# Kernel optimization log

Measured on AMD Instinct MI355X. Metric: run time of the kernel, lower is better.

Reference implementation:

```python
import jax, jax.numpy as jnp
import numpy as np

S1, S2, B, H, E, IN, OUT, NL = 8, 32, 256, 1024, 512, 2, 2, 4


def setup_inputs() -> dict:
    key = jax.random.key(0)
    ks = jax.random.split(key, 20)
    s_h = 1.0 / np.sqrt(H)
    inp = {
        'input': jax.random.normal(ks[0], (B, IN), jnp.float32),
        'h0': jax.random.normal(ks[1], (NL, B, H), jnp.float32) * 0.5,
        'c0': jax.random.normal(ks[2], (NL, B, H), jnp.float32) * 0.5,
        'all_outputs': jax.random.normal(ks[3], (S1, S2, B, H), jnp.float32),
        'W_emb': jax.random.normal(ks[4], (E, IN), jnp.float32) / np.sqrt(IN),
        'b_emb': jax.random.normal(ks[5], (E,), jnp.float32) * 0.01,
        'W_attn': jax.random.normal(ks[6], (1, 2 * H), jnp.float32) / np.sqrt(2 * H),
        'b_attn': jax.random.normal(ks[7], (1,), jnp.float32) * 0.01,
        'Wih0': jax.random.normal(ks[8], (4 * H, E + H), jnp.float32) / np.sqrt(E + H),
        'Whh0': jax.random.normal(ks[9], (4 * H, H), jnp.float32) * s_h,
        'bih0': jax.random.normal(ks[10], (4 * H,), jnp.float32) * 0.01,
        'bhh0': jax.random.normal(ks[11], (4 * H,), jnp.float32) * 0.01,
        'Wih_r': jax.random.normal(ks[12], (NL - 1, 4 * H, H), jnp.float32) * s_h,
        'Whh_r': jax.random.normal(ks[13], (NL - 1, 4 * H, H), jnp.float32) * s_h,
        'bih_r': jax.random.normal(ks[14], (NL - 1, 4 * H), jnp.float32) * 0.01,
        'bhh_r': jax.random.normal(ks[15], (NL - 1, 4 * H), jnp.float32) * 0.01,
        'W_out': jax.random.normal(ks[16], (OUT, H), jnp.float32) * s_h,
        'b_out': jax.random.normal(ks[17], (OUT,), jnp.float32) * 0.01,
    }
    return inp


def _lstm_cell(x, h, c, Wih, Whh, bih, bhh):
    g = x @ Wih.T + h @ Whh.T + bih + bhh  # [B, 4H], torch gate order i,f,g,o
    i, f, gg, o = jnp.split(g, 4, axis=1)
    c2 = jax.nn.sigmoid(f) * c + jax.nn.sigmoid(i) * jnp.tanh(gg)
    h2 = jax.nn.sigmoid(o) * jnp.tanh(c2)
    return h2, c2


def reference(input, h0, c0, all_outputs, W_emb, b_emb, W_attn, b_attn,
              Wih0, Whh0, bih0, bhh0, Wih_r, Whh_r, bih_r, bhh_r, W_out, b_out):
    s1, s2, b, h_dim = all_outputs.shape
    # embedding (dropout = identity in eval mode)
    embedded = jax.nn.relu(input @ W_emb.T + b_emb)  # [B, E]
    h_top = h0[0]  # [B, H]
    # attn(cat(h_top, y)) decomposed: h part is shared across all (j, i)
    w_h = W_attn[0, :h_dim]
    w_y = W_attn[0, h_dim:]
    scores = (jnp.einsum('jibh,h->jib', all_outputs, w_y)
              + (h_top @ w_h)[None, None, :] + b_attn[0])  # [S1, S2, B]
    # torch cats per-(j,i) [B,1] columns j-major -> [B, S1*S2]
    normalized = jax.nn.softmax(scores.reshape(s1 * s2, b).T, axis=1)  # [B, S1*S2]
    temp = normalized.reshape(b, s1, s2)
    # NOTE: original writes into an expand()-ed zero buffer, so every j-slice
    # aliases the same memory; after the loop all slices equal the last j's bmm
    # result and sum(0) multiplies it by S1. We replicate that exactly.
    applied_last = jnp.einsum('bi,ibh->bh', temp[:, -1, :], all_outputs[-1])  # [B, H]
    final_attn = s1 * applied_last
    x = jnp.concatenate([final_attn, embedded], axis=1)  # [B, H+E]
    hs, cs = [], []
    h, c = _lstm_cell(x, h0[0], c0[0], Wih0, Whh0, bih0, bhh0)
    hs.append(h); cs.append(c)
    for l in range(Wih_r.shape[0]):  # inter-layer dropout = identity in eval
        h, c = _lstm_cell(h, h0[l + 1], c0[l + 1], Wih_r[l], Whh_r[l], bih_r[l], bhh_r[l])
        hs.append(h); cs.append(c)
    h_new = jnp.stack(hs)
    c_new = jnp.stack(cs)
    final_output = h @ W_out.T + b_out  # [B, OUT]
    return final_output, h_new, c_new, normalized
```

## Files before the change

### kernel.cpp

```cpp
#include <hip/hip_runtime.h>
#include <hip/hip_bf16.h>

typedef __bf16 bf16x8 __attribute__((ext_vector_type(8)));
typedef __bf16 bf16x4 __attribute__((ext_vector_type(4)));
typedef float  f32x4  __attribute__((ext_vector_type(4)));

#define O_FINAL 0
#define O_H     512
#define O_C     1049088
#define O_NORM  2097664

__device__ __forceinline__ bf16x8 cvt8(float4 a, float4 b) {
  bf16x8 r;
  r[0] = (__bf16)a.x; r[1] = (__bf16)a.y; r[2] = (__bf16)a.z; r[3] = (__bf16)a.w;
  r[4] = (__bf16)b.x; r[5] = (__bf16)b.y; r[6] = (__bf16)b.z; r[7] = (__bf16)b.w;
  return r;
}

template<int K>
__device__ __forceinline__ void tile_gemm_bb(const __bf16* __restrict__ A,
                                             const __bf16* __restrict__ W,
                                             int r0, int j0, char* lds,
                                             f32x4 acc[2]) {
  constexpr int NK = K / 64;
  constexpr int D = 4;
  const int t = threadIdx.x, lane = t & 63, wave = t >> 6;
  const int rf = wave & 3, gg = wave >> 2;
  const int tr = t >> 3, chunk = t & 7;
  const __bf16* wsrc = W + (size_t)((tr >> 4) * 1024 + j0 + (tr & 15)) * K + chunk * 8;
  const __bf16* asrc = A + (size_t)(r0 + tr) * K + chunk * 8;
  const int sw_off = (chunk ^ (tr & 7)) << 4;
  const int woff = 8192 + tr * 128 + sw_off;
  const int aoff = tr * 128 + sw_off;
  const int a_tr  = rf * 16 + (lane & 15);
  const int w_tr0 = gg * 32 + (lane & 15);
  const int w_tr1 = w_tr0 + 16;
  const int ksel  = lane >> 4;

  bf16x8 wp[D], ap[D];
#pragma unroll
  for (int d = 0; d < D; ++d) {
    wp[d] = *(const bf16x8*)(wsrc + d * 64);
    ap[d] = *(const bf16x8*)(asrc + d * 64);
  }
#pragma unroll
  for (int s = 0; s < NK; ++s) {
    const int sl = s % D;
    char* buf = lds + (s & 1) * 16384;
    *(bf16x8*)(buf + aoff) = ap[sl];
    *(bf16x8*)(buf + woff) = wp[sl];
    if (s + D < NK) {
      wp[sl] = *(const bf16x8*)(wsrc + (s + D) * 64);
      ap[sl] = *(const bf16x8*)(asrc + (s + D) * 64);
    }
    __syncthreads();
#pragma unroll
    for (int s2 = 0; s2 < 2; ++s2) {
      const int chk = s2 * 4 + ksel;
      bf16x8 af  = *(const bf16x8*)(buf + a_tr * 128 + ((chk ^ (a_tr & 7)) << 4));
      bf16x8 wf0 = *(const bf16x8*)(buf + 8192 + w_tr0 * 128 + ((chk ^ (w_tr0 & 7)) << 4));
      bf16x8 wf1 = *(const bf16x8*)(buf + 8192 + w_tr1 * 128 + ((chk ^ (w_tr1 & 7)) << 4));
      acc[0] = __builtin_amdgcn_mfma_f32_16x16x32_bf16(af, wf0, acc[0], 0, 0, 0);
      acc[1] = __builtin_amdgcn_mfma_f32_16x16x32_bf16(af, wf1, acc[1], 0, 0, 0);
    }
  }
}

template<int K>
__device__ __forceinline__ void tile_gemm_ff(const float* __restrict__ A,
                                             const float* __restrict__ W,
                                             int r0, int j0, char* lds,
                                             f32x4 acc[2]) {
  constexpr int NK = K / 64;
  constexpr int D = 4;
  const int t = threadIdx.x, lane = t & 63, wave = t >> 6;
  const int rf = wave & 3, gg = wave >> 2;
  const int tr = t >> 3, chunk = t & 7;
  const float* wsrc = W + (size_t)((tr >> 4) * 1024 + j0 + (tr & 15)) * K + chunk * 8;
  const float* asrc = A + (size_t)(r0 + tr) * K + chunk * 8;
  const int sw_off = (chunk ^ (tr & 7)) << 4;
  const int woff = 8192 + tr * 128 + sw_off;
  const int aoff = tr * 128 + sw_off;
  const int a_tr  = rf * 16 + (lane & 15);
  const int w_tr0 = gg * 32 + (lane & 15);
  const int w_tr1 = w_tr0 + 16;
  const int ksel  = lane >> 4;

  float4 wp[D][2], ap[D][2];
#pragma unroll
  for (int d = 0; d < D; ++d) {
    wp[d][0] = *(const float4*)(wsrc + d * 64);
    wp[d][1] = *(const float4*)(wsrc + d * 64 + 4);
    ap[d][0] = *(const float4*)(asrc + d * 64);
    ap[d][1] = *(const float4*)(asrc + d * 64 + 4);
  }
#pragma unroll
  for (int s = 0; s < NK; ++s) {
    const int sl = s % D;
    char* buf = lds + (s & 1) * 16384;
    *(bf16x8*)(buf + aoff) = cvt8(ap[sl][0], ap[sl][1]);
    *(bf16x8*)(buf + woff) = cvt8(wp[sl][0], wp[sl][1]);
    if (s + D < NK) {
      wp[sl][0] = *(const float4*)(wsrc + (s + D) * 64);
      wp[sl][1] = *(const float4*)(wsrc + (s + D) * 64 + 4);
      ap[sl][0] = *(const float4*)(asrc + (s + D) * 64);
      ap[sl][1] = *(const float4*)(asrc + (s + D) * 64 + 4);
    }
    __syncthreads();
#pragma unroll
    for (int s2 = 0; s2 < 2; ++s2) {
      const int chk = s2 * 4 + ksel;
      bf16x8 af  = *(const bf16x8*)(buf + a_tr * 128 + ((chk ^ (a_tr & 7)) << 4));
      bf16x8 wf0 = *(const bf16x8*)(buf + 8192 + w_tr0 * 128 + ((chk ^ (w_tr0 & 7)) << 4));
      bf16x8 wf1 = *(const bf16x8*)(buf + 8192 + w_tr1 * 128 + ((chk ^ (w_tr1 & 7)) << 4));
      acc[0] = __builtin_amdgcn_mfma_f32_16x16x32_bf16(af, wf0, acc[0], 0, 0, 0);
      acc[1] = __builtin_amdgcn_mfma_f32_16x16x32_bf16(af, wf1, acc[1], 0, 0, 0);
    }
  }
}

__global__ __launch_bounds__(512) void k_front(
    const float* __restrict__ AO, const float* __restrict__ Wattn,
    float* __restrict__ sc,
    const float* __restrict__ h0,
    const float* __restrict__ Whh0, const float* __restrict__ Whh_r,
    const float* __restrict__ bih0, const float* __restrict__ bhh0,
    const float* __restrict__ bih_r, const float* __restrict__ bhh_r,
    float* __restrict__ Gh,
    const float* __restrict__ Wih0, const float* __restrict__ Wih_r,
    __bf16* __restrict__ Wihb) {
  const int t = threadIdx.x, lane = t & 63, wave = t >> 6;
  if (blockIdx.x < 2048) {
    const float* wy = Wattn + 1024;
    float4 wv[4];
#pragma unroll
    for (int q = 0; q < 4; ++q) wv[q] = *(const float4*)(wy + lane * 4 + 256 * q);
    const int row0 = (blockIdx.x * 8 + wave) * 4;
    float a4[4];
#pragma unroll
    for (int rr = 0; rr < 4; ++rr) {
      const float4* rp = (const float4*)(AO + (size_t)(row0 + rr) * 1024);
      float a = 0.f;
#pragma unroll
      for (int q = 0; q < 4; ++q) {
        float4 v = rp[lane + 64 * q];
        a += v.x * wv[q].x + v.y * wv[q].y + v.z * wv[q].z + v.w * wv[q].w;
      }
      a4[rr] = a;
    }
#pragma unroll
    for (int rr = 0; rr < 4; ++rr) {
      float a = a4[rr];
#pragma unroll
      for (int off = 32; off; off >>= 1) a += __shfl_xor(a, off, 64);
      if (lane == 0) {
        int row = row0 + rr;
        sc[(row & 255) * 256 + (row >> 8)] = a;
      }
    }
    return;
  }
  if (blockIdx.x < 3072) {
    __shared__ char smem[40960];
    const int j = blockIdx.x - 2048;
    const int l = j >> 8, inner = j & 255;
    const int cb = inner & 63, rb = inner >> 6;
    const int j0 = cb * 16, r0 = rb * 64;
    const float* A  = h0 + (size_t)l * 262144;
    const float* W  = (l == 0) ? Whh0 : (Whh_r + (size_t)(l - 1) * 4194304);
    const float* bi = (l == 0) ? bih0 : (bih_r + (size_t)(l - 1) * 4096);
    const float* bh = (l == 0) ? bhh0 : (bhh_r + (size_t)(l - 1) * 4096);
    f32x4 acc[2] = {};
    tile_gemm_ff<1024>(A, W, r0, j0, smem, acc);
    float* Go = Gh + (size_t)l * 1048576;
    const int rf = wave & 3, gg = wave >> 2;
    const int col = j0 + (lane & 15);
    const int rbase = r0 + rf * 16 + ((lane >> 4) << 2);
#pragma unroll
    for (int gi = 0; gi < 2; ++gi) {
      const int cg = (gg * 2 + gi) * 1024 + col;
#pragma unroll
      for (int q = 0; q < 4; ++q)
        Go[(size_t)(rbase + q) * 4096 + cg] = acc[gi][q] + bi[cg] + bh[cg];
    }
    return;
  }
  const int tid = ((int)blockIdx.x - 3072) * 512 + t;
#pragma unroll
  for (int n = 0; n < 8; ++n) {
    int idx = tid + n * 589824;
    float4 v = (idx < 1572864) ? ((const float4*)Wih0)[idx]
                               : ((const float4*)Wih_r)[idx - 1572864];
    bf16x4 o;
    o[0] = (__bf16)v.x; o[1] = (__bf16)v.y; o[2] = (__bf16)v.z; o[3] = (__bf16)v.w;
    ((bf16x4*)Wihb)[idx] = o;
  }
}

__global__ __launch_bounds__(256) void k_smx(const float* __restrict__ sc,
                                             const float* __restrict__ AO,
                                             const float* __restrict__ inp,
                                             const float* __restrict__ Wemb,
                                             const float* __restrict__ bemb,
                                             float* __restrict__ norm_out,
                                             __bf16* __restrict__ x) {
  __shared__ float red[4];
  __shared__ float wsm[32];
  const int b = blockIdx.x, t = threadIdx.x, lane = t & 63, wave = t >> 6;
  float s = sc[b * 256 + t];
  float m = s;
#pragma unroll
  for (int off = 32; off; off >>= 1) m = fmaxf(m, __shfl_xor(m, off, 64));
  if (lane == 0) red[wave] = m;
  __syncthreads();
  m = fmaxf(fmaxf(red[0], red[1]), fmaxf(red[2], red[3]));
  float e = __expf(s - m);
  float sum = e;
#pragma unroll
  for (int off = 32; off; off >>= 1) sum += __shfl_xor(sum, off, 64);
  __syncthreads();
  if (lane == 0) red[wave] = sum;
  __syncthreads();
  sum = red[0] + red[1] + red[2] + red[3];
  float nv = e / sum;
  norm_out[b * 256 + t] = nv;
  if (t >= 224) wsm[t - 224] = nv;
  __syncthreads();
  float acc[4] = {0.f, 0.f, 0.f, 0.f};
  const float* base = AO + ((size_t)224 * 256 + b) * 1024;
#pragma unroll 4
  for (int i = 0; i < 32; ++i) {
    float w = wsm[i];
    const float* rp = base + (size_t)i * 262144;
#pragma unroll
    for (int q = 0; q < 4; ++q) acc[q] += w * rp[t + 256 * q];
  }
#pragma unroll
  for (int q = 0; q < 4; ++q) x[(size_t)b * 1536 + t + 256 * q] = (__bf16)(8.0f * acc[q]);
  float i0 = inp[b * 2], i1 = inp[b * 2 + 1];
#pragma unroll
  for (int r = 0; r < 2; ++r) {
    int jj = t + 256 * r;
    float e2 = i0 * Wemb[jj * 2] + i1 * Wemb[jj * 2 + 1] + bemb[jj];
    x[(size_t)b * 1536 + 1024 + jj] = (__bf16)fmaxf(e2, 0.f);
  }
}

template<int K>
__global__ __launch_bounds__(512) void k_layer(const __bf16* __restrict__ A,
                                               const __bf16* __restrict__ Wb,
                                               const float* __restrict__ Gh,
                                               const float* __restrict__ c0l,
                                               float* __restrict__ h_out,
                                               float* __restrict__ c_out,
                                               __bf16* __restrict__ hb) {
  __shared__ char smem[40960];
  float* exch = (float*)(smem + 32768);
  const int t = threadIdx.x, lane = t & 63, wave = t >> 6;
  const int rf = wave & 3, gg = wave >> 2;
  const int cb = blockIdx.x & 63, rb = blockIdx.x >> 6;
  const int j0 = cb * 16, r0 = rb * 64;
  f32x4 acc[2] = {};
  tile_gemm_bb<K>(A, Wb, r0, j0, smem, acc);
  const int col = j0 + (lane & 15);
  const int rbase = r0 + rf * 16 + ((lane >> 4) << 2);
#pragma unroll
  for (int gi = 0; gi < 2; ++gi) {
    const float* gp = Gh + (size_t)rbase * 4096 + (gg * 2 + gi) * 1024 + col;
#pragma unroll
    for (int q = 0; q < 4; ++q) acc[gi][q] += gp[(size_t)q * 4096];
  }
  const int eidx = ((lane >> 4) << 2) * 16 + (lane & 15);
  __syncthreads();
  if (gg == 1) {
#pragma unroll
    for (int gi = 0; gi < 2; ++gi)
#pragma unroll
      for (int q = 0; q < 4; ++q)
        exch[(rf * 2 + gi) * 256 + eidx + q * 16] = acc[gi][q];
  }
  __syncthreads();
  if (gg == 0) {
#pragma unroll
    for (int q = 0; q < 4; ++q) {
      const int row = rbase + q;
      float gv = exch[(rf * 2 + 0) * 256 + eidx + q * 16];
      float ov = exch[(rf * 2 + 1) * 256 + eidx + q * 16];
      float si = 1.f / (1.f + __expf(-acc[0][q]));
      float sf = 1.f / (1.f + __expf(-acc[1][q]));
      float so = 1.f / (1.f + __expf(-ov));
      float c2 = sf * c0l[(size_t)row * 1024 + col] + si * tanhf(gv);
      float h2 = so * tanhf(c2);
      h_out[(size_t)row * 1024 + col] = h2;
      c_out[(size_t)row * 1024 + col] = c2;
      hb[(size_t)row * 1024 + col] = (__bf16)h2;
    }
  }
}

__global__ __launch_bounds__(256) void k_final(const float* __restrict__ h3,
                                               const float* __restrict__ Wout,
                                               const float* __restrict__ bout,
                                               float* __restrict__ out) {
  const int lane = threadIdx.x & 63, wave = threadIdx.x >> 6;
  const int b = blockIdx.x * 4 + wave;
  const float4* hp = (const float4*)(h3 + (size_t)b * 1024);
  const float4* w0 = (const float4*)Wout;
  const float4* w1 = (const float4*)(Wout + 1024);
  float a0 = 0.f, a1 = 0.f;
#pragma unroll
  for (int q = 0; q < 4; ++q) {
    float4 hv = hp[lane + 64 * q];
    float4 v0 = w0[lane + 64 * q];
    float4 v1 = w1[lane + 64 * q];
    a0 += hv.x * v0.x + hv.y * v0.y + hv.z * v0.z + hv.w * v0.w;
    a1 += hv.x * v1.x + hv.y * v1.y + hv.z * v1.z + hv.w * v1.w;
  }
#pragma unroll
  for (int off = 32; off; off >>= 1) {
    a0 += __shfl_xor(a0, off, 64);
    a1 += __shfl_xor(a1, off, 64);
  }
  if (lane == 0) {
    out[b * 2]     = a0 + bout[0];
    out[b * 2 + 1] = a1 + bout[1];
  }
}

extern "C" void kernel_launch(void* const* d_in, const int* in_sizes, int n_in,
                              void* d_out, int out_size, void* d_ws, size_t ws_size,
                              hipStream_t stream) {
  const float* inp    = (const float*)d_in[0];
  const float* h0     = (const float*)d_in[1];
  const float* c0     = (const float*)d_in[2];
  const float* AO     = (const float*)d_in[3];
  const float* Wemb   = (const float*)d_in[4];
  const float* bemb   = (const float*)d_in[5];
  const float* Wattn  = (const float*)d_in[6];
  const float* Wih0   = (const float*)d_in[8];
  const float* Whh0   = (const float*)d_in[9];
  const float* bih0   = (const float*)d_in[10];
  const float* bhh0   = (const float*)d_in[11];
  const float* Wih_r  = (const float*)d_in[12];
  const float* Whh_r  = (const float*)d_in[13];
  const float* bih_r  = (const float*)d_in[14];
  const float* bhh_r  = (const float*)d_in[15];
  const float* Wout   = (const float*)d_in[16];
  const float* bout   = (const float*)d_in[17];

  float* out = (float*)d_out;
  char* ws = (char*)d_ws;

  __bf16* Wihb  = (__bf16*)ws;
  float*  Gh    = (float*)(ws + 37748736);
  __bf16* xb    = (__bf16*)(ws + 54525952);
  __bf16* hb    = (__bf16*)(ws + 55312384);
  float*  sc    = (float*)(ws + 57409536);
  __bf16* Wihb0 = Wihb;
  __bf16* Wihbr = Wihb + 6291456;

  k_front<<<4224, 512, 0, stream>>>(AO, Wattn, sc, h0, Whh0, Whh_r,
                                    bih0, bhh0, bih_r, bhh_r, Gh,
                                    Wih0, Wih_r, Wihb);
  k_smx<<<256, 256, 0, stream>>>(sc, AO, inp, Wemb, bemb, out + O_NORM, xb);

  k_layer<1536><<<256, 512, 0, stream>>>(xb, Wihb0, Gh, c0,
                                         out + O_H, out + O_C, hb);
  for (int l = 1; l < 4; ++l)
    k_layer<1024><<<256, 512, 0, stream>>>(hb + (size_t)(l - 1) * 262144,
                                           Wihbr + (size_t)(l - 1) * 4194304,
                                           Gh + (size_t)l * 1048576,
                                           c0 + (size_t)l * 262144,
                                           out + O_H + (size_t)l * 262144,
                                           out + O_C + (size_t)l * 262144,
                                           hb + (size_t)l * 262144);

  k_final<<<64, 256, 0, stream>>>(out + O_H + 3 * 262144, Wout, bout, out + O_FINAL);
}
```

Baseline: 154.1 us.

## Fuse recurrent GEMM into layer kernels and read fp32 weights directly

Result: no change. 153.2 us (-0.6%).

```diff
diff --git a/kernel.cpp b/kernel.cpp
--- a/kernel.cpp
+++ b/kernel.cpp
@@ -2,7 +2,6 @@
 #include <hip/hip_bf16.h>
 
 typedef __bf16 bf16x8 __attribute__((ext_vector_type(8)));
-typedef __bf16 bf16x4 __attribute__((ext_vector_type(4)));
 typedef float  f32x4  __attribute__((ext_vector_type(4)));
 
 #define O_FINAL 0
@@ -18,8 +17,8 @@
 }
 
 template<int K>
-__device__ __forceinline__ void tile_gemm_bb(const __bf16* __restrict__ A,
-                                             const __bf16* __restrict__ W,
+__device__ __forceinline__ void tile_gemm_bf(const __bf16* __restrict__ A,
+                                             const float* __restrict__ W,
                                              int r0, int j0, char* lds,
                                              f32x4 acc[2]) {
   constexpr int NK = K / 64;
@@ -27,7 +26,7 @@
   const int t = threadIdx.x, lane = t & 63, wave = t >> 6;
   const int rf = wave & 3, gg = wave >> 2;
   const int tr = t >> 3, chunk = t & 7;
-  const __bf16* wsrc = W + (size_t)((tr >> 4) * 1024 + j0 + (tr & 15)) * K + chunk * 8;
+  const float*  wsrc = W + (size_t)((tr >> 4) * 1024 + j0 + (tr & 15)) * K + chunk * 8;
   const __bf16* asrc = A + (size_t)(r0 + tr) * K + chunk * 8;
   const int sw_off = (chunk ^ (tr & 7)) << 4;
   const int woff = 8192 + tr * 128 + sw_off;
@@ -37,21 +36,23 @@
   const int w_tr1 = w_tr0 + 16;
   const int ksel  = lane >> 4;
 
-  bf16x8 wp[D], ap[D];
+  float4 wp[D][2]; bf16x8 ap[D];
 #pragma unroll
   for (int d = 0; d < D; ++d) {
-    wp[d] = *(const bf16x8*)(wsrc + d * 64);
-    ap[d] = *(const bf16x8*)(asrc + d * 64);
+    wp[d][0] = *(const float4*)(wsrc + d * 64);
+    wp[d][1] = *(const float4*)(wsrc + d * 64 + 4);
+    ap[d]    = *(const bf16x8*)(asrc + d * 64);
   }
 #pragma unroll
   for (int s = 0; s < NK; ++s) {
     const int sl = s % D;
     char* buf = lds + (s & 1) * 16384;
     *(bf16x8*)(buf + aoff) = ap[sl];
-    *(bf16x8*)(buf + woff) = wp[sl];
+    *(bf16x8*)(buf + woff) = cvt8(wp[sl][0], wp[sl][1]);
     if (s + D < NK) {
-      wp[sl] = *(const bf16x8*)(wsrc + (s + D) * 64);
-      ap[sl] = *(const bf16x8*)(asrc + (s + D) * 64);
+      wp[sl][0] = *(const float4*)(wsrc + (s + D) * 64);
+      wp[sl][1] = *(const float4*)(wsrc + (s + D) * 64 + 4);
+      ap[sl]    = *(const bf16x8*)(asrc + (s + D) * 64);
     }
     __syncthreads();
 #pragma unroll
@@ -119,81 +120,36 @@
   }
 }
 
-__global__ __launch_bounds__(512) void k_front(
-    const float* __restrict__ AO, const float* __restrict__ Wattn,
-    float* __restrict__ sc,
-    const float* __restrict__ h0,
-    const float* __restrict__ Whh0, const float* __restrict__ Whh_r,
-    const float* __restrict__ bih0, const float* __restrict__ bhh0,
-    const float* __restrict__ bih_r, const float* __restrict__ bhh_r,
-    float* __restrict__ Gh,
-    const float* __restrict__ Wih0, const float* __restrict__ Wih_r,
-    __bf16* __restrict__ Wihb) {
-  const int t = threadIdx.x, lane = t & 63, wave = t >> 6;
-  if (blockIdx.x < 2048) {
-    const float* wy = Wattn + 1024;
-    float4 wv[4];
-#pragma unroll
-    for (int q = 0; q < 4; ++q) wv[q] = *(const float4*)(wy + lane * 4 + 256 * q);
-    const int row0 = (blockIdx.x * 8 + wave) * 4;
-    float a4[4];
-#pragma unroll
-    for (int rr = 0; rr < 4; ++rr) {
-      const float4* rp = (const float4*)(AO + (size_t)(row0 + rr) * 1024);
-      float a = 0.f;
-#pragma unroll
-      for (int q = 0; q < 4; ++q) {
-        float4 v = rp[lane + 64 * q];
-        a += v.x * wv[q].x + v.y * wv[q].y + v.z * wv[q].z + v.w * wv[q].w;
-      }
-      a4[rr] = a;
-    }
-#pragma unroll
-    for (int rr = 0; rr < 4; ++rr) {
-      float a = a4[rr];
-#pragma unroll
-      for (int off = 32; off; off >>= 1) a += __shfl_xor(a, off, 64);
-      if (lane == 0) {
-        int row = row0 + rr;
-        sc[(row & 255) * 256 + (row >> 8)] = a;
-      }
-    }
-    return;
-  }
-  if (blockIdx.x < 3072) {
-    __shared__ char smem[40960];
-    const int j = blockIdx.x - 2048;
-    const int l = j >> 8, inner = j & 255;
-    const int cb = inner & 63, rb = inner >> 6;
-    const int j0 = cb * 16, r0 = rb * 64;
-    const float* A  = h0 + (size_t)l * 262144;
-    const float* W  = (l == 0) ? Whh0 : (Whh_r + (size_t)(l - 1) * 4194304);
-    const float* bi = (l == 0) ? bih0 : (bih_r + (size_t)(l - 1) * 4096);
-    const float* bh = (l == 0) ? bhh0 : (bhh_r + (size_t)(l - 1) * 4096);
-    f32x4 acc[2] = {};
-    tile_gemm_ff<1024>(A, W, r0, j0, smem, acc);
-    float* Go = Gh + (size_t)l * 1048576;
-    const int rf = wave & 3, gg = wave >> 2;
-    const int col = j0 + (lane & 15);
-    const int rbase = r0 + rf * 16 + ((lane >> 4) << 2);
-#pragma unroll
-    for (int gi = 0; gi < 2; ++gi) {
-      const int cg = (gg * 2 + gi) * 1024 + col;
-#pragma unroll
-      for (int q = 0; q < 4; ++q)
-        Go[(size_t)(rbase + q) * 4096 + cg] = acc[gi][q] + bi[cg] + bh[cg];
-    }
-    return;
-  }
-  const int tid = ((int)blockIdx.x - 3072) * 512 + t;
-#pragma unroll
-  for (int n = 0; n < 8; ++n) {
-    int idx = tid + n * 589824;
-    float4 v = (idx < 1572864) ? ((const float4*)Wih0)[idx]
-                               : ((const float4*)Wih_r)[idx - 1572864];
-    bf16x4 o;
-    o[0] = (__bf16)v.x; o[1] = (__bf16)v.y; o[2] = (__bf16)v.z; o[3] = (__bf16)v.w;
-    ((bf16x4*)Wihb)[idx] = o;
+__global__ __launch_bounds__(512) void k_scores(const float* __restrict__ AO,
+                                                const float* __restrict__ Wattn,
+                                                float* __restrict__ sc) {
+  const int lane = threadIdx.x & 63, wave = threadIdx.x >> 6;
+  const float* wy = Wattn + 1024;
+  float4 wv[4];
+#pragma unroll
+  for (int q = 0; q < 4; ++q) wv[q] = *(const float4*)(wy + lane * 4 + 256 * q);
+  const int row0 = (blockIdx.x * 8 + wave) * 4;
+  float a4[4];
+#pragma unroll
+  for (int rr = 0; rr < 4; ++rr) {
+    const float4* rp = (const float4*)(AO + (size_t)(row0 + rr) * 1024);
+    float a = 0.f;
+#pragma unroll
+    for (int q = 0; q < 4; ++q) {
+      float4 v = rp[lane + 64 * q];
+      a += v.x * wv[q].x + v.y * wv[q].y + v.z * wv[q].z + v.w * wv[q].w;
+    }
+    a4[rr] = a;
+  }
+#pragma unroll
+  for (int rr = 0; rr < 4; ++rr) {
+    float a = a4[rr];
+#pragma unroll
+    for (int off = 32; off; off >>= 1) a += __shfl_xor(a, off, 64);
+    if (lane == 0) {
+      int row = row0 + rr;
+      sc[(row & 255) * 256 + (row >> 8)] = a;
+    }
   }
 }
 
@@ -246,10 +202,13 @@
   }
 }
 
-template<int K>
+template<int KA>
 __global__ __launch_bounds__(512) void k_layer(const __bf16* __restrict__ A,
-                                               const __bf16* __restrict__ Wb,
-                                               const float* __restrict__ Gh,
+                                               const float* __restrict__ Wih,
+                                               const float* __restrict__ h0l,
+                                               const float* __restrict__ Whh,
+                                               const float* __restrict__ bi,
+                                               const float* __restrict__ bh,
                                                const float* __restrict__ c0l,
                                                float* __restrict__ h_out,
                                                float* __restrict__ c_out,
@@ -261,17 +220,17 @@
   const int cb = blockIdx.x & 63, rb = blockIdx.x >> 6;
   const int j0 = cb * 16, r0 = rb * 64;
   f32x4 acc[2] = {};
-  tile_gemm_bb<K>(A, Wb, r0, j0, smem, acc);
+  tile_gemm_bf<KA>(A, Wih, r0, j0, smem, acc);
+  tile_gemm_ff<1024>(h0l, Whh, r0, j0, smem, acc);
   const int col = j0 + (lane & 15);
   const int rbase = r0 + rf * 16 + ((lane >> 4) << 2);
+  const int eidx = ((lane >> 4) << 2) * 16 + (lane & 15);
 #pragma unroll
   for (int gi = 0; gi < 2; ++gi) {
-    const float* gp = Gh + (size_t)rbase * 4096 + (gg * 2 + gi) * 1024 + col;
-#pragma unroll
-    for (int q = 0; q < 4; ++q) acc[gi][q] += gp[(size_t)q * 4096];
-  }
-  const int eidx = ((lane >> 4) << 2) * 16 + (lane & 15);
-  __syncthreads();
+    const int cg = (gg * 2 + gi) * 1024 + col;
+    const float bsum = bi[cg] + bh[cg];
+    acc[gi][0] += bsum; acc[gi][1] += bsum; acc[gi][2] += bsum; acc[gi][3] += bsum;
+  }
   if (gg == 1) {
 #pragma unroll
     for (int gi = 0; gi < 2; ++gi)
@@ -351,25 +310,22 @@
   float* out = (float*)d_out;
   char* ws = (char*)d_ws;
 
-  __bf16* Wihb  = (__bf16*)ws;
-  float*  Gh    = (float*)(ws + 37748736);
-  __bf16* xb    = (__bf16*)(ws + 54525952);
-  __bf16* hb    = (__bf16*)(ws + 55312384);
-  float*  sc    = (float*)(ws + 57409536);
-  __bf16* Wihb0 = Wihb;
-  __bf16* Wihbr = Wihb + 6291456;
-
-  k_front<<<4224, 512, 0, stream>>>(AO, Wattn, sc, h0, Whh0, Whh_r,
-                                    bih0, bhh0, bih_r, bhh_r, Gh,
-                                    Wih0, Wih_r, Wihb);
+  float*  sc = (float*)ws;
+  __bf16* xb = (__bf16*)(ws + 262144);
+  __bf16* hb = (__bf16*)(ws + 1048576);
+
+  k_scores<<<2048, 512, 0, stream>>>(AO, Wattn, sc);
   k_smx<<<256, 256, 0, stream>>>(sc, AO, inp, Wemb, bemb, out + O_NORM, xb);
 
-  k_layer<1536><<<256, 512, 0, stream>>>(xb, Wihb0, Gh, c0,
+  k_layer<1536><<<256, 512, 0, stream>>>(xb, Wih0, h0, Whh0, bih0, bhh0, c0,
                                          out + O_H, out + O_C, hb);
   for (int l = 1; l < 4; ++l)
     k_layer<1024><<<256, 512, 0, stream>>>(hb + (size_t)(l - 1) * 262144,
-                                           Wihbr + (size_t)(l - 1) * 4194304,
-                                           Gh + (size_t)l * 1048576,
+                                           Wih_r + (size_t)(l - 1) * 4194304,
+                                           h0 + (size_t)l * 262144,
+                                           Whh_r + (size_t)(l - 1) * 4194304,
+                                           bih_r + (size_t)(l - 1) * 4096,
+                                           bhh_r + (size_t)(l - 1) * 4096,
                                            c0 + (size_t)l * 262144,
                                            out + O_H + (size_t)l * 262144,
                                            out + O_C + (size_t)l * 262144,
```
